# Kernel optimization log

Measured on AMD Instinct MI355X. Metric: run time of the kernel, lower is better.

Reference implementation:

```python
import jax, jax.numpy as jnp
import numpy as np
import math

D_MODEL = 1024
HEADS = 16
D_K = D_MODEL // HEADS
NUM_TURNS = 30
VOCAB_B = NUM_TURNS ** 2  # 900


def setup_inputs() -> dict:
    key = jax.random.key(0)
    ks = jax.random.split(key, 16)
    bs, Lq, Lk = 4, 512, 2048
    q = jax.random.normal(ks[0], (bs, Lq, D_MODEL), jnp.float32)
    k = jax.random.normal(ks[1], (bs, Lk, D_MODEL), jnp.float32)
    v = jax.random.normal(ks[2], (bs, Lk, D_MODEL), jnp.float32)
    b_idx = jax.random.randint(ks[3], (bs, Lq, Lk), 0, VOCAB_B, jnp.int32)
    mask = jax.random.randint(ks[4], (bs, Lq, Lk), 0, 2, jnp.int32)
    s = 1.0 / math.sqrt(D_MODEL)
    Wq = jax.random.normal(ks[5], (D_MODEL, D_MODEL), jnp.float32) * s
    bq = jnp.zeros((D_MODEL,), jnp.float32)
    Wk = jax.random.normal(ks[6], (D_MODEL, D_MODEL), jnp.float32) * s
    bk = jnp.zeros((D_MODEL,), jnp.float32)
    Wv = jax.random.normal(ks[7], (D_MODEL, D_MODEL), jnp.float32) * s
    bv = jnp.zeros((D_MODEL,), jnp.float32)
    Wo = jax.random.normal(ks[8], (D_MODEL, D_MODEL), jnp.float32) * s
    bo = jnp.zeros((D_MODEL,), jnp.float32)
    # bias embedding table, padding_idx=0 -> zero row
    b_table = jax.random.normal(ks[9], (VOCAB_B, HEADS), jnp.float32) * 0.02
    b_table = b_table.at[0].set(0.0)
    return {"q": q, "k": k, "v": v, "b_idx": b_idx, "mask": mask,
            "Wq": Wq, "bq": bq, "Wk": Wk, "bk": bk, "Wv": Wv, "bv": bv,
            "Wo": Wo, "bo": bo, "b_table": b_table}


def reference(q, k, v, b_idx, mask, Wq, bq, Wk, bk, Wv, bv, Wo, bo, b_table):
    bs, Lq, _ = q.shape
    Lk = k.shape[1]
    # projections, reshape to (bs, h, L, d_k)
    qh = (q @ Wq.T + bq).reshape(bs, Lq, HEADS, D_K).transpose(0, 2, 1, 3)
    kh = (k @ Wk.T + bk).reshape(bs, Lk, HEADS, D_K).transpose(0, 2, 1, 3)
    vh = (v @ Wv.T + bv).reshape(bs, Lk, HEADS, D_K).transpose(0, 2, 1, 3)
    # learned additive bias: embedding lookup (bs,Lq,Lk,h) -> (bs,h,Lq,Lk)
    b = b_table[b_idx].transpose(0, 3, 1, 2)
    scores = jnp.einsum('bhqd,bhkd->bhqk', qh, kh) / math.sqrt(D_K) + b
    scores = jnp.where(mask[:, None] == 0, jnp.float32(-1e9), scores)
    attn = jax.nn.softmax(scores, axis=-1)
    out = jnp.einsum('bhqk,bhkd->bhqd', attn, vh)
    out = out.transpose(0, 2, 1, 3).reshape(bs, Lq, D_MODEL)
    return out @ Wo.T + bo
```

## Files before the change

### kernel.cpp

```cpp
#include <hip/hip_runtime.h>
#include <hip/hip_bf16.h>

#define H 16
#define DK 64
#define DM 1024
#define LQ 512
#define LK 2048
#define BSZ 4

typedef __hip_bfloat16 bf16;
typedef __attribute__((ext_vector_type(8))) short short8;
typedef __attribute__((ext_vector_type(4))) short short4v;
typedef __attribute__((ext_vector_type(4))) float f32x4;

#define LOG2E 1.44269504f
#define SC2 0.18033688f


__global__ __launch_bounds__(256) void fused_cvt(
    const float* __restrict__ q, const float* __restrict__ k, const float* __restrict__ v,
    const int* __restrict__ bidx, const int* __restrict__ msk,
    const float* __restrict__ Wq, const float* __restrict__ Wk,
    const float* __restrict__ Wv, const float* __restrict__ Wo,
    const float* __restrict__ btab,
    bf16* __restrict__ qb, bf16* __restrict__ kb, bf16* __restrict__ vb,
    bf16* __restrict__ Wqb, bf16* __restrict__ Wkb, bf16* __restrict__ Wvb,
    bf16* __restrict__ Wob, short* __restrict__ pkd, float* __restrict__ btabT) {
  const int blk = blockIdx.x, tid = threadIdx.x;
  const float* src;
  bf16* dst;
  int base;
  if (blk < 2048)       { src = q;  dst = qb;  base = blk; }
  else if (blk < 10240) { src = k;  dst = kb;  base = blk - 2048; }
  else if (blk < 18432) { src = v;  dst = vb;  base = blk - 10240; }
  else if (blk < 19456) { src = Wq; dst = Wqb; base = blk - 18432; }
  else if (blk < 20480) { src = Wk; dst = Wkb; base = blk - 19456; }
  else if (blk < 21504) { src = Wv; dst = Wvb; base = blk - 20480; }
  else if (blk < 22528) { src = Wo; dst = Wob; base = blk - 21504; }
  else if (blk < 26624) {
    int i = (blk - 22528) * 1024 + tid * 4;
    int4 a = *reinterpret_cast<const int4*>(bidx + i);
    int4 m = *reinterpret_cast<const int4*>(msk + i);
    short4 r;
    r.x = m.x ? (short)a.x : (short)900;
    r.y = m.y ? (short)a.y : (short)900;
    r.z = m.z ? (short)a.z : (short)900;
    r.w = m.w ? (short)a.w : (short)900;
    *reinterpret_cast<short4*>(pkd + i) = r;
    return;
  } else {
    for (int j = tid; j < H * 901; j += 256) {
      int hh = j / 901, i = j - hh * 901;
      btabT[j] = (i == 900) ? -1e9f : (btab[i * H + hh] - 10.0f) * LOG2E;
    }
    return;
  }
  int i = base * 1024 + tid * 4;
  float4 val = *reinterpret_cast<const float4*>(src + i);
  bf16 o0 = __float2bfloat16(val.x), o1 = __float2bfloat16(val.y);
  bf16 o2 = __float2bfloat16(val.z), o3 = __float2bfloat16(val.w);
  short4 pk;
  pk.x = *reinterpret_cast<short*>(&o0);
  pk.y = *reinterpret_cast<short*>(&o1);
  pk.z = *reinterpret_cast<short*>(&o2);
  pk.w = *reinterpret_cast<short*>(&o3);
  *reinterpret_cast<short4*>(reinterpret_cast<short*>(dst) + i) = pk;
}


__device__ __forceinline__ void g2lds16(const bf16* g, bf16* l) {
  __builtin_amdgcn_global_load_lds(
      (__attribute__((address_space(1))) void*)(g),
      (__attribute__((address_space(3))) void*)(l), 16, 0, 0);
}

template <int MODE, int TM>
__device__ __forceinline__ void gemm_body(bf16* __restrict__ As, bf16* __restrict__ Bs,
                                          const bf16* __restrict__ A,
                                          const bf16* __restrict__ B,
                                          const float* __restrict__ bias,
                                          void* __restrict__ out,
                                          int M, int N, int K, int Lrows,
                                          int bx, int by) {
  constexpr int NT = (TM == 128) ? 4 : 2;
  const int tid = threadIdx.x;
  const int wave = tid >> 6, lane = tid & 63;
  const int quad = lane >> 4, l15 = lane & 15;
  const int rowbase = (TM == 128) ? (wave >> 1) * 64 : 0;
  const int colbase = (TM == 128) ? (wave & 1) * 64 : wave * 32;
  const int rowA0 = bx * TM, colB0 = by * 128;
  const int sro = lane >> 3;
  const int sgs = ((lane & 7) - sro) & 7;

  f32x4 acc[4][NT];
  const f32x4 zero = {0.f, 0.f, 0.f, 0.f};
  for (int mt = 0; mt < 4; mt++)
    for (int nt = 0; nt < NT; nt++) acc[mt][nt] = zero;

  for (int k0 = 0; k0 < K; k0 += 64) {
    for (int c = 0; c < TM / 32; ++c) {
      int r = wave * (TM / 4) + c * 8;
      g2lds16(A + (size_t)(rowA0 + r + sro) * K + k0 + sgs * 8, As + r * 64);
    }
    for (int c = 0; c < 4; ++c) {
      int r = wave * 32 + c * 8;
      g2lds16(B + (size_t)(colB0 + r + sro) * K + k0 + sgs * 8, Bs + r * 64);
    }
    __syncthreads();
    for (int ks = 0; ks < 2; ++ks) {
      short8 af[4], bfr[NT];
      for (int mt = 0; mt < 4; mt++)
        af[mt] = *reinterpret_cast<const short8*>(
            As + (rowbase + mt * 16 + l15) * 64 + (((ks * 4 + quad + l15) & 7) << 3));
      for (int nt = 0; nt < NT; nt++)
        bfr[nt] = *reinterpret_cast<const short8*>(
            Bs + (colbase + nt * 16 + l15) * 64 + (((ks * 4 + quad + l15) & 7) << 3));
      for (int mt = 0; mt < 4; mt++)
        for (int nt = 0; nt < NT; nt++) {
          if (MODE == 1)
            acc[mt][nt] = __builtin_amdgcn_mfma_f32_16x16x32_bf16(bfr[nt], af[mt], acc[mt][nt], 0, 0, 0);
          else
            acc[mt][nt] = __builtin_amdgcn_mfma_f32_16x16x32_bf16(af[mt], bfr[nt], acc[mt][nt], 0, 0, 0);
        }
    }
    __syncthreads();
  }

  const int bb = (MODE == 2) ? 0 : (rowA0 / Lrows);
  const int lb = (MODE == 2) ? rowA0 : (rowA0 - bb * Lrows);
  if (MODE == 1) {
    for (int mt = 0; mt < 4; mt++) {
      int key = lb + rowbase + mt * 16 + l15;
      for (int nt = 0; nt < NT; nt++) {
        f32x4 v = acc[mt][nt];
        for (int r = 0; r < 4; r++) {
          int ncol = colB0 + colbase + nt * 16 + quad * 4 + r;
          float bv = bias[ncol];
          int hh = ncol >> 6, d = ncol & 63;
          ((bf16*)out)[((size_t)((bb * H + hh) * DK + d)) * LK + key] =
              __float2bfloat16(v[r] + bv);
        }
      }
    }
    return;
  }
  for (int nt = 0; nt < NT; nt++) {
    int col = colB0 + colbase + nt * 16 + l15;
    float bv = bias[col];
    int hh = col >> 6, d = col & 63;
    for (int mt = 0; mt < 4; mt++) {
      int lrow0 = lb + rowbase + mt * 16 + quad * 4;
      f32x4 v = acc[mt][nt];
      for (int r = 0; r < 4; r++) {
        float val = v[r] + bv;
        if (MODE == 0) {
          ((bf16*)out)[(((size_t)(bb * H + hh) * Lrows + lrow0 + r) << 6) + d] = __float2bfloat16(val);
        } else {
          ((float*)out)[(size_t)(lrow0 + r) * N + col] = val;
        }
      }
    }
  }
}

__global__ __launch_bounds__(256) void proj_qkv(
    const bf16* __restrict__ kb, const bf16* __restrict__ Wkb, const float* __restrict__ bk, bf16* __restrict__ Kh,
    const bf16* __restrict__ vb, const bf16* __restrict__ Wvb, const float* __restrict__ bv, bf16* __restrict__ Vt,
    const bf16* __restrict__ qb, const bf16* __restrict__ Wqb, const float* __restrict__ bq, bf16* __restrict__ Qh) {
  __shared__ __align__(16) bf16 As[128 * 64];
  __shared__ __align__(16) bf16 Bs[128 * 64];
  const int blk = blockIdx.x;
  if (blk < 512) {
    const int xcd = blk & 7, slot = blk >> 3;
    gemm_body<0, 128>(As, Bs, kb, Wkb, bk, (void*)Kh, 8192, 1024, 1024, LK,
                      xcd * 8 + (slot & 7), slot >> 3);
  } else if (blk < 1024) {
    const int i = blk - 512, xcd = i & 7, slot = i >> 3;
    gemm_body<1, 128>(As, Bs, vb, Wvb, bv, (void*)Vt, 8192, 1024, 1024, LK,
                      xcd * 8 + (slot & 7), slot >> 3);
  } else {
    const int i = blk - 1024, xcd = i & 7, slot = i >> 3;
    gemm_body<0, 64>(As, Bs, qb, Wqb, bq, (void*)Qh, 2048, 1024, 1024, LQ,
                     xcd * 4 + (slot & 3), slot >> 2);
  }
}

__global__ __launch_bounds__(256) void gemm_o(const bf16* __restrict__ A,
                                              const bf16* __restrict__ B,
                                              const float* __restrict__ bias,
                                              float* __restrict__ out) {
  __shared__ __align__(16) bf16 As[64 * 64];
  __shared__ __align__(16) bf16 Bs[128 * 64];
  const int blk = blockIdx.x, xcd = blk & 7, slot = blk >> 3;
  gemm_body<2, 64>(As, Bs, A, B, bias, (void*)out, 2048, 1024, 1024, LQ,
                   xcd * 4 + (slot & 3), slot >> 2);
}


__global__ __launch_bounds__(512) void attn9(const bf16* __restrict__ Qh,
                                             const bf16* __restrict__ Kh,
                                             const bf16* __restrict__ Vt,
                                             const short* __restrict__ pkm,
                                             const float* __restrict__ btabT,
                                             float* __restrict__ Opart,
                                             float* __restrict__ L) {
  __shared__ __align__(16) bf16 Kbuf[2][64 * 64];
  __shared__ __align__(16) bf16 Vbuf[2][64 * 64];
  __shared__ float bts[901];
  const int tid = threadIdx.x;
  const int wave = tid >> 6, lane = tid & 63;
  const int quad = lane >> 4, l15 = lane & 15;
  const int bh = blockIdx.x, b = bh >> 4, h = bh & 15;
  const int qt = blockIdx.y, z = blockIdx.z;
  const int key_base = z * 1024;

  for (int i = tid; i < 901; i += 512) bts[i] = btabT[h * 901 + i];

  const int q = qt * 128 + wave * 16 + l15;
  short8 qf[2];
  for (int ks = 0; ks < 2; ks++)
    qf[ks] = *reinterpret_cast<const short8*>(
        Qh + ((size_t)bh * LQ + q) * DK + ks * 32 + quad * 8);

  const bf16* kbase = Kh + ((size_t)bh * LK + key_base) * DK;
  const bf16* vbase = Vt + ((size_t)bh * DK) * LK + key_base;
  const short* pkrow = pkm + ((size_t)b * LQ + q) * LK + key_base;

  const int srow_off = lane >> 3;
  const int sseg = ((lane & 7) - srow_off) & 7;
  const int srow = wave * 8 + srow_off;

  f32x4 of[4];
  float denom = 0.f;
  const f32x4 zero = {0.f, 0.f, 0.f, 0.f};
  for (int dt = 0; dt < 4; dt++) of[dt] = zero;

  g2lds16(kbase + (size_t)srow * DK + sseg * 8, &Kbuf[0][(wave * 8) * 64]);
  g2lds16(vbase + (size_t)srow * LK + sseg * 8, &Vbuf[0][(wave * 8) * 64]);
  short4v pkv[4];
  for (int nt = 0; nt < 4; nt++)
    pkv[nt] = *reinterpret_cast<const short4v*>(pkrow + nt * 16 + quad * 4);

  __syncthreads();

  for (int kc = 0; kc < 16; ++kc) {
    const int buf = kc & 1;

    short4v pk_n[4];
    if (kc < 15) {
      const int key1 = (kc + 1) * 64;
      g2lds16(kbase + (size_t)(key1 + srow) * DK + sseg * 8,
              &Kbuf[buf ^ 1][(wave * 8) * 64]);
      g2lds16(vbase + (size_t)srow * LK + key1 + sseg * 8,
              &Vbuf[buf ^ 1][(wave * 8) * 64]);
      for (int nt = 0; nt < 4; nt++)
        pk_n[nt] = *reinterpret_cast<const short4v*>(pkrow + key1 + nt * 16 + quad * 4);
    }

    f32x4 sa[4];
    for (int nt = 0; nt < 4; nt++) sa[nt] = zero;
    for (int nt = 0; nt < 4; nt++)
      for (int ks = 0; ks < 2; ks++) {
        short8 kf = *reinterpret_cast<const short8*>(
            &Kbuf[buf][(nt * 16 + l15) * 64 + (((ks * 4 + quad + l15) & 7) << 3)]);
        sa[nt] = __builtin_amdgcn_mfma_f32_16x16x32_bf16(kf, qf[ks], sa[nt], 0, 0, 0);
      }

    short4v vf[4][4];
    for (int dt = 0; dt < 4; dt++)
      for (int nt = 0; nt < 4; nt++)
        vf[dt][nt] = *reinterpret_cast<const short4v*>(
            &Vbuf[buf][(dt * 16 + l15) * 64 +
                       (((nt * 2 + (quad >> 1) + l15) & 7) << 3) + ((quad & 1) << 2)]);

    short4v pf[4];
    for (int nt = 0; nt < 4; nt++) {
      float p[4];
      for (int r = 0; r < 4; r++) {
        float t = fmaf(sa[nt][r], SC2, bts[pkv[nt][r]]);
        p[r] = __builtin_amdgcn_exp2f(t);
      }
      denom += (p[0] + p[1]) + (p[2] + p[3]);
      short4v pk4;
      for (int r = 0; r < 4; r++) {
        bf16 tb = __float2bfloat16(p[r]);
        pk4[r] = *reinterpret_cast<short*>(&tb);
      }
      pf[nt] = pk4;
    }

    for (int dt = 0; dt < 4; dt++)
      for (int nt = 0; nt < 4; nt++)
        of[dt] = __builtin_amdgcn_mfma_f32_16x16x16bf16_1k(vf[dt][nt], pf[nt], of[dt], 0, 0, 0);

    if (kc < 15)
      for (int nt = 0; nt < 4; nt++) pkv[nt] = pk_n[nt];

    __syncthreads();
  }

  denom += __shfl_xor(denom, 16, 64);
  denom += __shfl_xor(denom, 32, 64);

  size_t rowi = ((size_t)z * 64 + bh) * LQ + q;
  float* orow = Opart + rowi * 64;
  for (int dt = 0; dt < 4; dt++)
    *reinterpret_cast<f32x4*>(orow + dt * 16 + quad * 4) = of[dt];
  if (quad == 0) L[rowi] = denom;
}

__global__ __launch_bounds__(256) void attn_combine(const float* __restrict__ Opart,
                                                    const float* __restrict__ L,
                                                    bf16* __restrict__ Ob) {
  int t = blockIdx.x * 256 + threadIdx.x;
  int g = t * 4;
  int row = g >> 6, d0 = g & 63;
  float l = L[row] + L[32768 + row];
  float4 o;
  float4 p0 = *reinterpret_cast<const float4*>(Opart + ((size_t)row << 6) + d0);
  float4 p1 = *reinterpret_cast<const float4*>(Opart + (((size_t)32768 + row) << 6) + d0);
  o.x = p0.x + p1.x; o.y = p0.y + p1.y; o.z = p0.z + p1.z; o.w = p0.w + p1.w;
  float inv = 1.f / l;
  bf16 t0 = __float2bfloat16(o.x * inv), t1 = __float2bfloat16(o.y * inv);
  bf16 t2 = __float2bfloat16(o.z * inv), t3 = __float2bfloat16(o.w * inv);
  short4 pk;
  pk.x = *reinterpret_cast<short*>(&t0);
  pk.y = *reinterpret_cast<short*>(&t1);
  pk.z = *reinterpret_cast<short*>(&t2);
  pk.w = *reinterpret_cast<short*>(&t3);
  int bh = row >> 9, qq = row & 511, b_ = bh >> 4, h = bh & 15;
  *reinterpret_cast<short4*>(Ob + ((size_t)(b_ * LQ + qq)) * DM + h * 64 + d0) = pk;
}


extern "C" void kernel_launch(void* const* d_in, const int* in_sizes, int n_in,
                              void* d_out, int out_size, void* d_ws, size_t ws_size,
                              hipStream_t stream) {
  const float* q = (const float*)d_in[0];
  const float* k = (const float*)d_in[1];
  const float* v = (const float*)d_in[2];
  const int* bidx = (const int*)d_in[3];
  const int* mask = (const int*)d_in[4];
  const float* Wq = (const float*)d_in[5];
  const float* bq = (const float*)d_in[6];
  const float* Wk = (const float*)d_in[7];
  const float* bk = (const float*)d_in[8];
  const float* Wv = (const float*)d_in[9];
  const float* bv = (const float*)d_in[10];
  const float* Wo = (const float*)d_in[11];
  const float* bo = (const float*)d_in[12];
  const float* btab = (const float*)d_in[13];

  char* ws = (char*)d_ws;
  bf16* qb  = (bf16*)(ws + 0);
  bf16* kb  = (bf16*)(ws + 4194304);
  bf16* vb  = (bf16*)(ws + 20971520);
  bf16* Wqb = (bf16*)(ws + 37748736);
  bf16* Wkb = (bf16*)(ws + 39845888);
  bf16* Wvb = (bf16*)(ws + 41943040);
  bf16* Wob = (bf16*)(ws + 44040192);
  bf16* Qh  = (bf16*)(ws + 46137344);
  bf16* Kh  = (bf16*)(ws + 50331648);
  bf16* Vt  = (bf16*)(ws + 67108864);
  short* pkd = (short*)(ws + 83886080);
  bf16* Ob  = (bf16*)(ws + 92274688);
  float* btabT = (float*)(ws + 92274688);
  float* Opart = (float*)(ws + 0);
  float* L     = (float*)(ws + 16777216);
  (void)ws_size; (void)in_sizes; (void)n_in; (void)out_size;

  hipLaunchKernelGGL(fused_cvt, dim3(26625), dim3(256), 0, stream,
                     q, k, v, bidx, mask, Wq, Wk, Wv, Wo, btab,
                     qb, kb, vb, Wqb, Wkb, Wvb, Wob, pkd, btabT);

  hipLaunchKernelGGL(proj_qkv, dim3(1280), dim3(256), 0, stream,
                     kb, Wkb, bk, Kh, vb, Wvb, bv, Vt, qb, Wqb, bq, Qh);

  hipLaunchKernelGGL(attn9, dim3(BSZ * H, LQ / 128, 2), dim3(512), 0, stream,
                     Qh, Kh, Vt, pkd, btabT, Opart, L);
  hipLaunchKernelGGL(attn_combine, dim3(2048), dim3(256), 0, stream,
                     Opart, L, Ob);

  hipLaunchKernelGGL(gemm_o, dim3(256), dim3(256), 0, stream,
                     Ob, Wob, bo, (float*)d_out);
}
```

Baseline: 297.7 us.

## Drop split-key attention and fuse normalization into single-pass attention kernel

The attention kernel no longer splits the 2048 keys into two halves with a separate combine kernel. Each block now walks all 32 key chunks, then normalizes by the row denominator and writes bf16 output directly in the layout gemm_o expects. This removes the fp32 partial-output and denominator writes, their re-read, and one kernel launch. The cost is half as many blocks (256 instead of 512), which gives less parallelism and weaker latency hiding per CU, and a longer serial loop per block.

After: 320.2 us. +7.6%, slower.

```diff
diff --git a/kernel.cpp b/kernel.cpp
--- a/kernel.cpp
+++ b/kernel.cpp
@@ -197,13 +197,12 @@
 }
 
 
-__global__ __launch_bounds__(512) void attn9(const bf16* __restrict__ Qh,
-                                             const bf16* __restrict__ Kh,
-                                             const bf16* __restrict__ Vt,
-                                             const short* __restrict__ pkm,
-                                             const float* __restrict__ btabT,
-                                             float* __restrict__ Opart,
-                                             float* __restrict__ L) {
+__global__ __launch_bounds__(512) void attn11(const bf16* __restrict__ Qh,
+                                              const bf16* __restrict__ Kh,
+                                              const bf16* __restrict__ Vt,
+                                              const short* __restrict__ pkm,
+                                              const float* __restrict__ btabT,
+                                              bf16* __restrict__ Ob) {
   __shared__ __align__(16) bf16 Kbuf[2][64 * 64];
   __shared__ __align__(16) bf16 Vbuf[2][64 * 64];
   __shared__ float bts[901];
@@ -211,8 +210,7 @@
   const int wave = tid >> 6, lane = tid & 63;
   const int quad = lane >> 4, l15 = lane & 15;
   const int bh = blockIdx.x, b = bh >> 4, h = bh & 15;
-  const int qt = blockIdx.y, z = blockIdx.z;
-  const int key_base = z * 1024;
+  const int qt = blockIdx.y;
 
   for (int i = tid; i < 901; i += 512) bts[i] = btabT[h * 901 + i];
 
@@ -222,9 +220,9 @@
     qf[ks] = *reinterpret_cast<const short8*>(
         Qh + ((size_t)bh * LQ + q) * DK + ks * 32 + quad * 8);
 
-  const bf16* kbase = Kh + ((size_t)bh * LK + key_base) * DK;
-  const bf16* vbase = Vt + ((size_t)bh * DK) * LK + key_base;
-  const short* pkrow = pkm + ((size_t)b * LQ + q) * LK + key_base;
+  const bf16* kbase = Kh + (size_t)bh * LK * DK;
+  const bf16* vbase = Vt + (size_t)bh * DK * LK;
+  const short* pkrow = pkm + ((size_t)b * LQ + q) * LK;
 
   const int srow_off = lane >> 3;
   const int sseg = ((lane & 7) - srow_off) & 7;
@@ -243,11 +241,11 @@
 
   __syncthreads();
 
-  for (int kc = 0; kc < 16; ++kc) {
+  for (int kc = 0; kc < 32; ++kc) {
     const int buf = kc & 1;
 
     short4v pk_n[4];
-    if (kc < 15) {
+    if (kc < 31) {
       const int key1 = (kc + 1) * 64;
       g2lds16(kbase + (size_t)(key1 + srow) * DK + sseg * 8,
               &Kbuf[buf ^ 1][(wave * 8) * 64]);
@@ -293,7 +291,7 @@
       for (int nt = 0; nt < 4; nt++)
         of[dt] = __builtin_amdgcn_mfma_f32_16x16x16bf16_1k(vf[dt][nt], pf[nt], of[dt], 0, 0, 0);
 
-    if (kc < 15)
+    if (kc < 31)
       for (int nt = 0; nt < 4; nt++) pkv[nt] = pk_n[nt];
 
     __syncthreads();
@@ -301,35 +299,21 @@
 
   denom += __shfl_xor(denom, 16, 64);
   denom += __shfl_xor(denom, 32, 64);
-
-  size_t rowi = ((size_t)z * 64 + bh) * LQ + q;
-  float* orow = Opart + rowi * 64;
-  for (int dt = 0; dt < 4; dt++)
-    *reinterpret_cast<f32x4*>(orow + dt * 16 + quad * 4) = of[dt];
-  if (quad == 0) L[rowi] = denom;
-}
-
-__global__ __launch_bounds__(256) void attn_combine(const float* __restrict__ Opart,
-                                                    const float* __restrict__ L,
-                                                    bf16* __restrict__ Ob) {
-  int t = blockIdx.x * 256 + threadIdx.x;
-  int g = t * 4;
-  int row = g >> 6, d0 = g & 63;
-  float l = L[row] + L[32768 + row];
-  float4 o;
-  float4 p0 = *reinterpret_cast<const float4*>(Opart + ((size_t)row << 6) + d0);
-  float4 p1 = *reinterpret_cast<const float4*>(Opart + (((size_t)32768 + row) << 6) + d0);
-  o.x = p0.x + p1.x; o.y = p0.y + p1.y; o.z = p0.z + p1.z; o.w = p0.w + p1.w;
-  float inv = 1.f / l;
-  bf16 t0 = __float2bfloat16(o.x * inv), t1 = __float2bfloat16(o.y * inv);
-  bf16 t2 = __float2bfloat16(o.z * inv), t3 = __float2bfloat16(o.w * inv);
-  short4 pk;
-  pk.x = *reinterpret_cast<short*>(&t0);
-  pk.y = *reinterpret_cast<short*>(&t1);
-  pk.z = *reinterpret_cast<short*>(&t2);
-  pk.w = *reinterpret_cast<short*>(&t3);
-  int bh = row >> 9, qq = row & 511, b_ = bh >> 4, h = bh & 15;
-  *reinterpret_cast<short4*>(Ob + ((size_t)(b_ * LQ + qq)) * DM + h * 64 + d0) = pk;
+  const float inv = 1.f / denom;
+
+  bf16* orow = Ob + ((size_t)(b * LQ + q)) * DM + h * 64;
+  for (int dt = 0; dt < 4; dt++) {
+    short4 pk;
+    bf16 t0 = __float2bfloat16(of[dt][0] * inv);
+    bf16 t1 = __float2bfloat16(of[dt][1] * inv);
+    bf16 t2 = __float2bfloat16(of[dt][2] * inv);
+    bf16 t3 = __float2bfloat16(of[dt][3] * inv);
+    pk.x = *reinterpret_cast<short*>(&t0);
+    pk.y = *reinterpret_cast<short*>(&t1);
+    pk.z = *reinterpret_cast<short*>(&t2);
+    pk.w = *reinterpret_cast<short*>(&t3);
+    *reinterpret_cast<short4*>(orow + dt * 16 + quad * 4) = pk;
+  }
 }
 
 
@@ -363,10 +347,8 @@
   bf16* Kh  = (bf16*)(ws + 50331648);
   bf16* Vt  = (bf16*)(ws + 67108864);
   short* pkd = (short*)(ws + 83886080);
-  bf16* Ob  = (bf16*)(ws + 92274688);
   float* btabT = (float*)(ws + 92274688);
-  float* Opart = (float*)(ws + 0);
-  float* L     = (float*)(ws + 16777216);
+  bf16* Ob = (bf16*)(ws + 0);
   (void)ws_size; (void)in_sizes; (void)n_in; (void)out_size;
 
   hipLaunchKernelGGL(fused_cvt, dim3(26625), dim3(256), 0, stream,
@@ -376,10 +358,8 @@
   hipLaunchKernelGGL(proj_qkv, dim3(1280), dim3(256), 0, stream,
                      kb, Wkb, bk, Kh, vb, Wvb, bv, Vt, qb, Wqb, bq, Qh);
 
-  hipLaunchKernelGGL(attn9, dim3(BSZ * H, LQ / 128, 2), dim3(512), 0, stream,
-                     Qh, Kh, Vt, pkd, btabT, Opart, L);
-  hipLaunchKernelGGL(attn_combine, dim3(2048), dim3(256), 0, stream,
-                     Opart, L, Ob);
+  hipLaunchKernelGGL(attn11, dim3(BSZ * H, LQ / 128), dim3(512), 0, stream,
+                     Qh, Kh, Vt, pkd, btabT, Ob);
 
   hipLaunchKernelGGL(gemm_o, dim3(256), dim3(256), 0, stream,
                      Ob, Wob, bo, (float*)d_out);
```
